# Optimization experiments

Measured on AMD Instinct MI355X. Metric: run time of the kernel, lower is better.

The kernel has to match this reference:

```python
import jax, jax.numpy as jnp
import numpy as np

N_NODES = 100000
N_EDGES = 3200000
F_IN, HIDDEN, N_CLASSES = 512, 256, 40


def setup_inputs() -> dict:
    key = jax.random.key(0)
    ks = jax.random.split(key, 8)
    x = jax.random.normal(ks[0], (N_NODES, F_IN), dtype=jnp.float32)
    edge_row = jax.random.randint(ks[1], (N_EDGES,), 0, N_NODES, dtype=jnp.int64)
    edge_col = jax.random.randint(ks[2], (N_EDGES,), 0, N_NODES, dtype=jnp.int64)
    edge_val = jax.random.uniform(ks[3], (N_EDGES,), dtype=jnp.float32)
    # Xavier-uniform-ish weights
    lim1 = float(np.sqrt(6.0 / (F_IN + HIDDEN)))
    lim2 = float(np.sqrt(6.0 / (HIDDEN + N_CLASSES)))
    W1 = jax.random.uniform(ks[4], (F_IN, HIDDEN), minval=-lim1, maxval=lim1, dtype=jnp.float32)
    b1 = jnp.zeros((HIDDEN,), dtype=jnp.float32)
    W2 = jax.random.uniform(ks[5], (HIDDEN, N_CLASSES), minval=-lim2, maxval=lim2, dtype=jnp.float32)
    b2 = jnp.zeros((N_CLASSES,), dtype=jnp.float32)
    return {"x": x, "edge_row": edge_row, "edge_col": edge_col, "edge_val": edge_val,
            "W1": W1, "b1": b1, "W2": W2, "b2": b2}


def _spmm(edge_row, edge_col, edge_val, h):
    # out[r] = sum_e val[e] * h[col[e]] for edges with row[e]==r  (a @ h)
    msg = edge_val[:, None] * h[edge_col]            # [E, F] gather + scale
    return jax.ops.segment_sum(msg, edge_row, num_segments=N_NODES)


def reference(x, edge_row, edge_col, edge_val, W1, b1, W2, b2):
    # Layer 1: dense mm -> spmm -> bias -> relu (dropout in eval mode = identity)
    h = _spmm(edge_row, edge_col, edge_val, x @ W1) + b1
    h = jax.nn.relu(h)
    # Layer 2: dense mm -> spmm -> bias
    logits = _spmm(edge_row, edge_col, edge_val, h @ W2) + b2
    return jax.nn.log_softmax(logits, axis=1)
```

## Files before the change

kernel.cpp:

```cpp
#include <hip/hip_runtime.h>
#include <math.h>

#define NN  100000
#define NE  3200000
#define FIN 512
#define HID 256
#define NC  40

#define NBUK 391
#define SPB  9472
#define BIN_BLOCKS 782
#define CHUNK 4096
#define COLMASK 0x1FFFF

typedef __attribute__((ext_vector_type(8))) short short8;
typedef __attribute__((ext_vector_type(4))) float f32x4;

__device__ inline float bf2f(unsigned short u) {
    unsigned int x = ((unsigned int)u) << 16;
    return __builtin_bit_cast(float, x);
}
__device__ inline unsigned short f2bfu(float f) {
    unsigned int x = __builtin_bit_cast(unsigned int, f);
    unsigned int r = (x + 0x7fffu + ((x >> 16) & 1u)) >> 16;
    return (unsigned short)r;
}
__device__ inline signed char q8(float v, float s) {
    int q = (int)rintf(v * s);
    q = max(-127, min(127, q));
    return (signed char)q;
}
__device__ inline unsigned cvtpk_bf16(float lo, float hi) {
    unsigned r;
    asm("v_cvt_pk_bf16_f32 %0, %1, %2" : "=v"(r) : "v"(lo), "v"(hi));
    return r;
}
__device__ inline float cub0(int r) { float f; asm("v_cvt_f32_ubyte0 %0, %1" : "=v"(f) : "v"(r)); return f; }
__device__ inline float cub1(int r) { float f; asm("v_cvt_f32_ubyte1 %0, %1" : "=v"(f) : "v"(r)); return f; }
__device__ inline float cub2(int r) { float f; asm("v_cvt_f32_ubyte2 %0, %1" : "=v"(f) : "v"(r)); return f; }
__device__ inline float cub3(int r) { float f; asm("v_cvt_f32_ubyte3 %0, %1" : "=v"(f) : "v"(r)); return f; }

__global__ __launch_bounds__(256) void k_prep(const float* __restrict__ W1, unsigned short* __restrict__ W1T,
                                              const float* __restrict__ W2, unsigned short* __restrict__ W2T,
                                              int* __restrict__ bcnt) {
    const int b = blockIdx.x;
    const int tid = threadIdx.x;
    if (b < 32) {
        unsigned short tmp[16];
#pragma unroll
        for (int kk = 0; kk < 16; kk++)
            tmp[kk] = f2bfu(W1[(size_t)(b * 16 + kk) * HID + tid]);
        unsigned short* dst = W1T + (size_t)tid * FIN + b * 16;
        *(short8*)dst = *(short8*)tmp;
        *(short8*)(dst + 8) = *(short8*)(tmp + 8);
    } else if (b < 80) {
        int n = b - 32;
        float v = (n < NC) ? W2[(size_t)tid * NC + n] : 0.f;
        W2T[(size_t)n * HID + tid] = f2bfu(v);
    } else {
        for (int i = tid; i < NBUK; i += 256) bcnt[i] = 0;
    }
}

__global__ __launch_bounds__(256) void k_bin(const int* __restrict__ er, const int* __restrict__ ec,
                                             const float* __restrict__ ev, int* __restrict__ bcnt,
                                             int2* __restrict__ spack) {
    __shared__ int hist[392];
    __shared__ int lscan[392];
    __shared__ int gbase[NBUK];
    __shared__ int lcur[NBUK];
    __shared__ int sm[256];
    __shared__ int2 ebuf[CHUNK];
    __shared__ unsigned short bbuf[CHUNK];
    const int tid = threadIdx.x;
    for (int i = tid; i < 392; i += 256) hist[i] = 0;
    for (int i = tid; i < NBUK; i += 256) lcur[i] = 0;
    __syncthreads();
    const int start = blockIdx.x * CHUNK;
    const int end = min(start + CHUNK, NE);
    const int n = end - start;
    for (int e = start + tid; e < end; e += 256)
        atomicAdd(&hist[er[e] >> 8], 1);
    __syncthreads();
    int a = (2 * tid < 392) ? hist[2 * tid] : 0;
    int b = (2 * tid + 1 < 392) ? hist[2 * tid + 1] : 0;
    int v = a + b;
    sm[tid] = v;
    __syncthreads();
    for (int off = 1; off < 256; off <<= 1) {
        int t2 = (tid >= off) ? sm[tid - off] : 0;
        __syncthreads();
        sm[tid] += t2;
        __syncthreads();
    }
    int ex = sm[tid] - v;
    if (2 * tid < 392) lscan[2 * tid] = ex;
    if (2 * tid + 1 < 392) lscan[2 * tid + 1] = ex + a;
    for (int i = tid; i < NBUK; i += 256) {
        int h = hist[i];
        gbase[i] = h ? atomicAdd(&bcnt[i], h) : 0;
    }
    __syncthreads();
    for (int e = start + tid; e < end; e += 256) {
        int r = er[e];
        int bk = r >> 8;
        int lpos = atomicAdd(&lcur[bk], 1);
        int pos = lscan[bk] + lpos;
        int2 p;
        p.x = ((r & 255) << 17) | ec[e];
        p.y = __builtin_bit_cast(int, ev[e]);
        ebuf[pos] = p;
        bbuf[pos] = (unsigned short)bk;
    }
    __syncthreads();
    for (int i = tid; i < n; i += 256) {
        int bk = bbuf[i];
        spack[(size_t)bk * SPB + gbase[bk] + (i - lscan[bk])] = ebuf[i];
    }
}

__global__ __launch_bounds__(256) void k_finecsr(const int2* __restrict__ spack, const int* __restrict__ bcnt,
                                                 int2* __restrict__ cpack,
                                                 int* __restrict__ row_beg, int* __restrict__ row_cnt) {
    __shared__ int cnt[256];
    __shared__ int sm[256];
    __shared__ int cur[256];
    int tid = threadIdx.x;
    int buk = blockIdx.x;
    size_t bb = (size_t)buk * SPB;
    int n = min(bcnt[buk], SPB);
    cnt[tid] = 0;
    __syncthreads();
    for (int i = tid; i < n; i += 256) {
        int lr = ((unsigned)spack[bb + i].x) >> 17;
        atomicAdd(&cnt[lr], 1);
    }
    __syncthreads();
    int v = cnt[tid];
    sm[tid] = v;
    __syncthreads();
    for (int off = 1; off < 256; off <<= 1) {
        int t = (tid >= off) ? sm[tid - off] : 0;
        __syncthreads();
        sm[tid] += t;
        __syncthreads();
    }
    int ex = sm[tid] - v;
    cur[tid] = ex;
    int grow = buk * 256 + tid;
    if (grow < NN) {
        row_beg[grow] = (int)bb + ex;
        row_cnt[grow] = v;
    }
    __syncthreads();
    for (int i = tid; i < n; i += 256) {
        int2 p = spack[bb + i];
        int lr = ((unsigned)p.x) >> 17;
        int pos = atomicAdd(&cur[lr], 1);
        int2 q;
        q.x = p.x & COLMASK;
        q.y = p.y;
        cpack[bb + pos] = q;
    }
}

__global__ __launch_bounds__(256, 4) void k_gemm1(const float* __restrict__ x, const unsigned short* __restrict__ W1T,
                                                  unsigned char* __restrict__ h1) {
    __shared__ unsigned short As[64][40];
    __shared__ unsigned short Bs[128][40];
    const int tid = threadIdx.x;
    const int row0 = (blockIdx.x >> 1) * 64;
    const int col0 = (blockIdx.x & 1) * 128;
    const int lane = tid & 63;
    const int w = tid >> 6;
    const int wr = (w >> 1) * 32;
    const int wc = (w & 1) * 64;
    const int m16 = lane & 15;
    const int quad = lane >> 4;

    const int arow = tid >> 2;
    const int akoff = (tid & 3) * 8;
    int gar = row0 + arow;
    if (gar >= NN) gar = NN - 1;
    const float* ax = x + (size_t)gar * FIN + akoff;
    const int brow = tid >> 1;
    const int bkoff = (tid & 1) * 16;
    const unsigned short* bw = W1T + (size_t)(col0 + brow) * FIN + bkoff;

    f32x4 acc[2][4];
#pragma unroll
    for (int i = 0; i < 2; i++)
#pragma unroll
        for (int j = 0; j < 4; j++) acc[i][j] = (f32x4){0.f, 0.f, 0.f, 0.f};

    float4 va0, va1;
    uint4 vb0, vb1;

#define G1_LOAD(tt)                                                        \
    {                                                                      \
        const float* ap = ax + (tt) * 32;                                  \
        va0 = *(const float4*)(ap);                                        \
        va1 = *(const float4*)(ap + 4);                                    \
        const unsigned short* bp = bw + (tt) * 32;                         \
        vb0 = *(const uint4*)(bp);                                         \
        vb1 = *(const uint4*)(bp + 8);                                     \
    }

#define G1_STORE()                                                         \
    {                                                                      \
        uint4 pa;                                                          \
        pa.x = cvtpk_bf16(va0.x, va0.y);                                   \
        pa.y = cvtpk_bf16(va0.z, va0.w);                                   \
        pa.z = cvtpk_bf16(va1.x, va1.y);                                   \
        pa.w = cvtpk_bf16(va1.z, va1.w);                                   \
        *(uint4*)(&As[arow][akoff]) = pa;                                  \
        *(uint4*)(&Bs[brow][bkoff]) = vb0;                                 \
        *(uint4*)(&Bs[brow][bkoff + 8]) = vb1;                             \
    }

    G1_LOAD(0)
    G1_STORE()
    __syncthreads();

    for (int t = 0; t < 16; ++t) {
        if (t < 15) G1_LOAD(t + 1)
        short8 af[2], bfr[4];
#pragma unroll
        for (int i = 0; i < 2; i++) af[i] = *(const short8*)(&As[wr + i * 16 + m16][quad * 8]);
#pragma unroll
        for (int j = 0; j < 4; j++) bfr[j] = *(const short8*)(&Bs[wc + j * 16 + m16][quad * 8]);
#pragma unroll
        for (int i = 0; i < 2; i++)
#pragma unroll
            for (int j = 0; j < 4; j++)
                acc[i][j] = __builtin_amdgcn_mfma_f32_16x16x32_bf16(af[i], bfr[j], acc[i][j], 0, 0, 0);
        if (t < 15) {
            __syncthreads();
            G1_STORE()
            __syncthreads();
        }
    }
#undef G1_LOAD
#undef G1_STORE

#pragma unroll
    for (int i = 0; i < 2; i++) {
#pragma unroll
        for (int r = 0; r < 4; r++) {
            int gr = row0 + wr + i * 16 + quad * 4 + r;
            if (gr < NN) {
#pragma unroll
                for (int j = 0; j < 4; j++) {
                    int c = col0 + wc + j * 16 + m16;
                    h1[(size_t)gr * HID + c] = (unsigned char)(q8(acc[i][j][r], 16.f) + 128);
                }
            }
        }
    }
}

__global__ __launch_bounds__(256) void k_spmm1(const unsigned char* __restrict__ h1,
                                               const int2* __restrict__ cpack,
                                               const int* __restrict__ row_beg, const int* __restrict__ row_cnt,
                                               const float* __restrict__ b1, unsigned short* __restrict__ a1) {
    const int lane = threadIdx.x & 63;
    const int row = (int)__builtin_amdgcn_readfirstlane(blockIdx.x * 4 + (threadIdx.x >> 6));
    if (row >= NN) return;
    const int beg = (int)__builtin_amdgcn_readfirstlane(row_beg[row]);
    const int cnt = (int)__builtin_amdgcn_readfirstlane(row_cnt[row]);
    const int end = beg + cnt;
    const int voff = lane * 4;
    float su[4] = {0.f, 0.f, 0.f, 0.f};
    float sv = 0.f;

    for (int e0 = beg; e0 < end; e0 += 16) {
        int2 p[16];
#pragma unroll
        for (int j = 0; j < 16; j++)
            p[j] = cpack[e0 + j];
        unsigned cb[16];
        float vv[16];
#pragma unroll
        for (int j = 0; j < 16; j++) {
            cb[j] = ((unsigned)p[j].x & COLMASK) << 8;
            vv[j] = (e0 + j) < end ? __builtin_bit_cast(float, p[j].y) : 0.f;
        }
        int g[16];
#pragma unroll
        for (int j = 0; j < 16; j++)
            g[j] = *(const int*)(h1 + (size_t)cb[j] + voff);
#pragma unroll
        for (int j = 0; j < 16; j++) {
            sv += vv[j];
            su[0] = fmaf(vv[j], cub0(g[j]), su[0]);
            su[1] = fmaf(vv[j], cub1(g[j]), su[1]);
            su[2] = fmaf(vv[j], cub2(g[j]), su[2]);
            su[3] = fmaf(vv[j], cub3(g[j]), su[3]);
        }
    }

    const int col = lane * 4;
    const float4 bb = *(const float4*)(b1 + col);
    ushort4 o;
    o.x = f2bfu(fmaxf(fmaf(0.0625f, fmaf(-128.f, sv, su[0]), bb.x), 0.f));
    o.y = f2bfu(fmaxf(fmaf(0.0625f, fmaf(-128.f, sv, su[1]), bb.y), 0.f));
    o.z = f2bfu(fmaxf(fmaf(0.0625f, fmaf(-128.f, sv, su[2]), bb.z), 0.f));
    o.w = f2bfu(fmaxf(fmaf(0.0625f, fmaf(-128.f, sv, su[3]), bb.w), 0.f));
    *(ushort4*)(a1 + (size_t)row * HID + col) = o;
}

__global__ __launch_bounds__(256) void k_gemm2(const unsigned short* __restrict__ a1,
                                               const unsigned short* __restrict__ W2T, unsigned char* __restrict__ h2) {
    const int tid = threadIdx.x;
    const int lane = tid & 63;
    const int w = tid >> 6;
    const int m16 = lane & 15;
    const int quad = lane >> 4;
    const int r0 = blockIdx.x * 256 + w * 64;

    f32x4 acc[4][3];
#pragma unroll
    for (int i = 0; i < 4; i++)
#pragma unroll
        for (int j = 0; j < 3; j++) acc[i][j] = (f32x4){0.f, 0.f, 0.f, 0.f};

    for (int k0 = 0; k0 < HID; k0 += 32) {
        short8 af[4], bfr[3];
#pragma unroll
        for (int i = 0; i < 4; i++) {
            int gr = r0 + i * 16 + m16;
            if (gr >= NN) gr = NN - 1;
            af[i] = *(const short8*)(a1 + (size_t)gr * HID + k0 + quad * 8);
        }
#pragma unroll
        for (int j = 0; j < 3; j++)
            bfr[j] = *(const short8*)(W2T + (size_t)(j * 16 + m16) * HID + k0 + quad * 8);
#pragma unroll
        for (int i = 0; i < 4; i++)
#pragma unroll
            for (int j = 0; j < 3; j++)
                acc[i][j] = __builtin_amdgcn_mfma_f32_16x16x32_bf16(af[i], bfr[j], acc[i][j], 0, 0, 0);
    }
#pragma unroll
    for (int i = 0; i < 4; i++) {
#pragma unroll
        for (int r = 0; r < 4; r++) {
            int gr = r0 + i * 16 + quad * 4 + r;
            if (gr < NN) {
#pragma unroll
                for (int j = 0; j < 3; j++) {
                    int c = j * 16 + m16;
                    if (c < NC) h2[(size_t)gr * 64 + c] = (unsigned char)(q8(acc[i][j][r], 4.f) + 128);
                }
            }
        }
    }
}

__global__ __launch_bounds__(256) void k_spmm2(const unsigned char* __restrict__ h2,
                                               const int2* __restrict__ cpack,
                                               const int* __restrict__ row_beg, const int* __restrict__ row_cnt,
                                               const float* __restrict__ b2, float* __restrict__ out) {
    const int lane = threadIdx.x & 63;
    const int slot = lane >> 4;
    const int t = lane & 15;
    const int row = (int)__builtin_amdgcn_readfirstlane(blockIdx.x * 4 + (threadIdx.x >> 6));
    if (row >= NN) return;
    const int beg = (int)__builtin_amdgcn_readfirstlane(row_beg[row]);
    const int cnt = (int)__builtin_amdgcn_readfirstlane(row_cnt[row]);
    const int end = beg + cnt;
    const int t4 = t * 4;
    float su[4] = {0.f, 0.f, 0.f, 0.f};
    float sv = 0.f;

    for (int e0 = beg; e0 < end; e0 += 32) {
        unsigned cb[8];
        float vs[8];
#pragma unroll
        for (int u = 0; u < 8; u++) {
            int idx = e0 + u * 4 + slot;
            int2 p = cpack[idx];
            cb[u] = ((unsigned)p.x & COLMASK) << 6;
            vs[u] = idx < end ? __builtin_bit_cast(float, p.y) : 0.f;
        }
        int g[8];
#pragma unroll
        for (int u = 0; u < 8; u++)
            g[u] = *(const int*)(h2 + (size_t)cb[u] + t4);
#pragma unroll
        for (int u = 0; u < 8; u++) {
            sv += vs[u];
            su[0] = fmaf(vs[u], cub0(g[u]), su[0]);
            su[1] = fmaf(vs[u], cub1(g[u]), su[1]);
            su[2] = fmaf(vs[u], cub2(g[u]), su[2]);
            su[3] = fmaf(vs[u], cub3(g[u]), su[3]);
        }
    }

#pragma unroll
    for (int i = 0; i < 4; i++) {
        su[i] += __shfl_xor(su[i], 16, 64);
        su[i] += __shfl_xor(su[i], 32, 64);
    }
    sv += __shfl_xor(sv, 16, 64);
    sv += __shfl_xor(sv, 32, 64);

    const bool act = t < 10;
    const int off = t4;
    const int boff = act ? off : 0;
    const float4 bb = *(const float4*)(b2 + boff);
    float acc[4];
    acc[0] = fmaf(0.25f, fmaf(-128.f, sv, su[0]), bb.x);
    acc[1] = fmaf(0.25f, fmaf(-128.f, sv, su[1]), bb.y);
    acc[2] = fmaf(0.25f, fmaf(-128.f, sv, su[2]), bb.z);
    acc[3] = fmaf(0.25f, fmaf(-128.f, sv, su[3]), bb.w);
    float mx = act ? fmaxf(fmaxf(acc[0], acc[1]), fmaxf(acc[2], acc[3])) : -INFINITY;
#pragma unroll
    for (int o = 1; o < 16; o <<= 1) mx = fmaxf(mx, __shfl_xor(mx, o, 16));
    float se = 0.f;
    if (act) {
#pragma unroll
        for (int i = 0; i < 4; i++) se += expf(acc[i] - mx);
    }
#pragma unroll
    for (int o = 1; o < 16; o <<= 1) se += __shfl_xor(se, o, 16);
    const float ls = logf(se);
    if (act && slot == 0) {
        float4 r;
        r.x = acc[0] - mx - ls;
        r.y = acc[1] - mx - ls;
        r.z = acc[2] - mx - ls;
        r.w = acc[3] - mx - ls;
        *(float4*)(out + (size_t)row * NC + off) = r;
    }
}

extern "C" void kernel_launch(void* const* d_in, const int* in_sizes, int n_in, void* d_out, int out_size,
                              void* d_ws, size_t ws_size, hipStream_t stream) {
    const float* x  = (const float*)d_in[0];
    const int*   er = (const int*)d_in[1];
    const int*   ec = (const int*)d_in[2];
    const float* ev = (const float*)d_in[3];
    const float* W1 = (const float*)d_in[4];
    const float* b1 = (const float*)d_in[5];
    const float* W2 = (const float*)d_in[6];
    const float* b2 = (const float*)d_in[7];
    float* out = (float*)d_out;
    char* ws = (char*)d_ws;

    int2*  spack       = (int2*)(ws + 0);
    unsigned char* h1  = (unsigned char*)(ws + 0);
    unsigned short* a1 = (unsigned short*)(ws + 29628416);
    unsigned char* h2  = (unsigned char*)(ws + 80828416);
    int2*  cpack       = (int2*)(ws + 87228416);
    int*   row_beg     = (int*)(ws + 116856832);
    int*   row_cnt     = (int*)(ws + 117256832);
    int*   bcnt        = (int*)(ws + 117656832);
    unsigned short* W1T = (unsigned short*)(ws + 117658880);
    unsigned short* W2T = (unsigned short*)(ws + 117921024);

    k_prep<<<81, 256, 0, stream>>>(W1, W1T, W2, W2T, bcnt);
    k_bin<<<BIN_BLOCKS, 256, 0, stream>>>(er, ec, ev, bcnt, spack);
    k_finecsr<<<NBUK, 256, 0, stream>>>(spack, bcnt, cpack, row_beg, row_cnt);
    k_gemm1<<<3126, 256, 0, stream>>>(x, W1T, h1);
    k_spmm1<<<NN / 4, 256, 0, stream>>>(h1, cpack, row_beg, row_cnt, b1, a1);
    k_gemm2<<<(NN + 255) / 256, 256, 0, stream>>>(a1, W2T, h2);
    k_spmm2<<<NN / 4, 256, 0, stream>>>(h2, cpack, row_beg, row_cnt, b2, out);
}
```

Before: 673.1 us.

## Fuse edge binning and GEMM1 into one launch with register-direct MFMA tiles

```diff
diff --git a/kernel.cpp b/kernel.cpp
--- a/kernel.cpp
+++ b/kernel.cpp
@@ -12,6 +12,7 @@
 #define BIN_BLOCKS 782
 #define CHUNK 4096
 #define COLMASK 0x1FFFF
+#define G1_BLOCKS 1563
 
 typedef __attribute__((ext_vector_type(8))) short short8;
 typedef __attribute__((ext_vector_type(4))) float f32x4;
@@ -62,60 +63,129 @@
     }
 }
 
-__global__ __launch_bounds__(256) void k_bin(const int* __restrict__ er, const int* __restrict__ ec,
-                                             const float* __restrict__ ev, int* __restrict__ bcnt,
-                                             int2* __restrict__ spack) {
-    __shared__ int hist[392];
-    __shared__ int lscan[392];
-    __shared__ int gbase[NBUK];
-    __shared__ int lcur[NBUK];
-    __shared__ int sm[256];
-    __shared__ int2 ebuf[CHUNK];
-    __shared__ unsigned short bbuf[CHUNK];
+__global__ __launch_bounds__(256) void k_fused(const float* __restrict__ x, const unsigned short* __restrict__ W1T,
+                                               unsigned char* __restrict__ h1,
+                                               const int* __restrict__ er, const int* __restrict__ ec,
+                                               const float* __restrict__ ev, int* __restrict__ bcnt,
+                                               int2* __restrict__ spack) {
     const int tid = threadIdx.x;
-    for (int i = tid; i < 392; i += 256) hist[i] = 0;
-    for (int i = tid; i < NBUK; i += 256) lcur[i] = 0;
-    __syncthreads();
-    const int start = blockIdx.x * CHUNK;
-    const int end = min(start + CHUNK, NE);
-    const int n = end - start;
-    for (int e = start + tid; e < end; e += 256)
-        atomicAdd(&hist[er[e] >> 8], 1);
-    __syncthreads();
-    int a = (2 * tid < 392) ? hist[2 * tid] : 0;
-    int b = (2 * tid + 1 < 392) ? hist[2 * tid + 1] : 0;
-    int v = a + b;
-    sm[tid] = v;
-    __syncthreads();
-    for (int off = 1; off < 256; off <<= 1) {
-        int t2 = (tid >= off) ? sm[tid - off] : 0;
-        __syncthreads();
-        sm[tid] += t2;
-        __syncthreads();
-    }
-    int ex = sm[tid] - v;
-    if (2 * tid < 392) lscan[2 * tid] = ex;
-    if (2 * tid + 1 < 392) lscan[2 * tid + 1] = ex + a;
-    for (int i = tid; i < NBUK; i += 256) {
-        int h = hist[i];
-        gbase[i] = h ? atomicAdd(&bcnt[i], h) : 0;
-    }
-    __syncthreads();
-    for (int e = start + tid; e < end; e += 256) {
-        int r = er[e];
-        int bk = r >> 8;
-        int lpos = atomicAdd(&lcur[bk], 1);
-        int pos = lscan[bk] + lpos;
-        int2 p;
-        p.x = ((r & 255) << 17) | ec[e];
-        p.y = __builtin_bit_cast(int, ev[e]);
-        ebuf[pos] = p;
-        bbuf[pos] = (unsigned short)bk;
-    }
-    __syncthreads();
-    for (int i = tid; i < n; i += 256) {
-        int bk = bbuf[i];
-        spack[(size_t)bk * SPB + gbase[bk] + (i - lscan[bk])] = ebuf[i];
+    if (blockIdx.x < BIN_BLOCKS) {
+        __shared__ int hist[392];
+        __shared__ int lscan[392];
+        __shared__ int gbase[NBUK];
+        __shared__ int lcur[NBUK];
+        __shared__ int sm[256];
+        __shared__ int2 ebuf[CHUNK];
+        __shared__ unsigned short bbuf[CHUNK];
+        for (int i = tid; i < 392; i += 256) hist[i] = 0;
+        for (int i = tid; i < NBUK; i += 256) lcur[i] = 0;
+        __syncthreads();
+        const int start = blockIdx.x * CHUNK;
+        const int end = min(start + CHUNK, NE);
+        const int n = end - start;
+        for (int e = start + tid; e < end; e += 256)
+            atomicAdd(&hist[er[e] >> 8], 1);
+        __syncthreads();
+        int a = (2 * tid < 392) ? hist[2 * tid] : 0;
+        int b = (2 * tid + 1 < 392) ? hist[2 * tid + 1] : 0;
+        int v = a + b;
+        sm[tid] = v;
+        __syncthreads();
+        for (int off = 1; off < 256; off <<= 1) {
+            int t2 = (tid >= off) ? sm[tid - off] : 0;
+            __syncthreads();
+            sm[tid] += t2;
+            __syncthreads();
+        }
+        int ex = sm[tid] - v;
+        if (2 * tid < 392) lscan[2 * tid] = ex;
+        if (2 * tid + 1 < 392) lscan[2 * tid + 1] = ex + a;
+        for (int i = tid; i < NBUK; i += 256) {
+            int h = hist[i];
+            gbase[i] = h ? atomicAdd(&bcnt[i], h) : 0;
+        }
+        __syncthreads();
+        for (int e = start + tid; e < end; e += 256) {
+            int r = er[e];
+            int bk = r >> 8;
+            int lpos = atomicAdd(&lcur[bk], 1);
+            int pos = lscan[bk] + lpos;
+            int2 p;
+            p.x = ((r & 255) << 17) | ec[e];
+            p.y = __builtin_bit_cast(int, ev[e]);
+            ebuf[pos] = p;
+            bbuf[pos] = (unsigned short)bk;
+        }
+        __syncthreads();
+        for (int i = tid; i < n; i += 256) {
+            int bk = bbuf[i];
+            spack[(size_t)bk * SPB + gbase[bk] + (i - lscan[bk])] = ebuf[i];
+        }
+        return;
+    }
+
+    const int gid = blockIdx.x - BIN_BLOCKS;
+    const int row0 = gid * 64;
+    const int lane = tid & 63;
+    const int w = tid >> 6;
+    const int col0 = w * 64;
+    const int m16 = lane & 15;
+    const int quad = lane >> 4;
+
+    const float* ap[4];
+#pragma unroll
+    for (int i = 0; i < 4; i++) {
+        int gr = row0 + i * 16 + m16;
+        if (gr >= NN) gr = NN - 1;
+        ap[i] = x + (size_t)gr * FIN + quad * 8;
+    }
+    const unsigned short* bp[4];
+#pragma unroll
+    for (int j = 0; j < 4; j++)
+        bp[j] = W1T + (size_t)(col0 + j * 16 + m16) * FIN + quad * 8;
+
+    f32x4 acc[4][4];
+#pragma unroll
+    for (int i = 0; i < 4; i++)
+#pragma unroll
+        for (int j = 0; j < 4; j++) acc[i][j] = (f32x4){0.f, 0.f, 0.f, 0.f};
+
+    for (int k0 = 0; k0 < FIN; k0 += 32) {
+        short8 af[4], bfr[4];
+#pragma unroll
+        for (int i = 0; i < 4; i++) {
+            const float4 lo = *(const float4*)(ap[i] + k0);
+            const float4 hi = *(const float4*)(ap[i] + k0 + 4);
+            uint4 pk;
+            pk.x = cvtpk_bf16(lo.x, lo.y);
+            pk.y = cvtpk_bf16(lo.z, lo.w);
+            pk.z = cvtpk_bf16(hi.x, hi.y);
+            pk.w = cvtpk_bf16(hi.z, hi.w);
+            af[i] = __builtin_bit_cast(short8, pk);
+        }
+#pragma unroll
+        for (int j = 0; j < 4; j++)
+            bfr[j] = *(const short8*)(bp[j] + k0);
+#pragma unroll
+        for (int i = 0; i < 4; i++)
+#pragma unroll
+            for (int j = 0; j < 4; j++)
+                acc[i][j] = __builtin_amdgcn_mfma_f32_16x16x32_bf16(af[i], bfr[j], acc[i][j], 0, 0, 0);
+    }
+
+#pragma unroll
+    for (int i = 0; i < 4; i++) {
+#pragma unroll
+        for (int r = 0; r < 4; r++) {
+            int gr = row0 + i * 16 + quad * 4 + r;
+            if (gr < NN) {
+#pragma unroll
+                for (int j = 0; j < 4; j++) {
+                    int c = col0 + j * 16 + m16;
+                    h1[(size_t)gr * HID + c] = (unsigned char)(q8(acc[i][j][r], 16.f) + 128);
+                }
+            }
+        }
     }
 }
 
@@ -164,101 +234,6 @@
     }
 }
 
-__global__ __launch_bounds__(256, 4) void k_gemm1(const float* __restrict__ x, const unsigned short* __restrict__ W1T,
-                                                  unsigned char* __restrict__ h1) {
-    __shared__ unsigned short As[64][40];
-    __shared__ unsigned short Bs[128][40];
-    const int tid = threadIdx.x;
-    const int row0 = (blockIdx.x >> 1) * 64;
-    const int col0 = (blockIdx.x & 1) * 128;
-    const int lane = tid & 63;
-    const int w = tid >> 6;
-    const int wr = (w >> 1) * 32;
-    const int wc = (w & 1) * 64;
-    const int m16 = lane & 15;
-    const int quad = lane >> 4;
-
-    const int arow = tid >> 2;
-    const int akoff = (tid & 3) * 8;
-    int gar = row0 + arow;
-    if (gar >= NN) gar = NN - 1;
-    const float* ax = x + (size_t)gar * FIN + akoff;
-    const int brow = tid >> 1;
-    const int bkoff = (tid & 1) * 16;
-    const unsigned short* bw = W1T + (size_t)(col0 + brow) * FIN + bkoff;
-
-    f32x4 acc[2][4];
-#pragma unroll
-    for (int i = 0; i < 2; i++)
-#pragma unroll
-        for (int j = 0; j < 4; j++) acc[i][j] = (f32x4){0.f, 0.f, 0.f, 0.f};
-
-    float4 va0, va1;
-    uint4 vb0, vb1;
-
-#define G1_LOAD(tt)                                                        \
-    {                                                                      \
-        const float* ap = ax + (tt) * 32;                                  \
-        va0 = *(const float4*)(ap);                                        \
-        va1 = *(const float4*)(ap + 4);                                    \
-        const unsigned short* bp = bw + (tt) * 32;                         \
-        vb0 = *(const uint4*)(bp);                                         \
-        vb1 = *(const uint4*)(bp + 8);                                     \
-    }
-
-#define G1_STORE()                                                         \
-    {                                                                      \
-        uint4 pa;                                                          \
-        pa.x = cvtpk_bf16(va0.x, va0.y);                                   \
-        pa.y = cvtpk_bf16(va0.z, va0.w);                                   \
-        pa.z = cvtpk_bf16(va1.x, va1.y);                                   \
-        pa.w = cvtpk_bf16(va1.z, va1.w);                                   \
-        *(uint4*)(&As[arow][akoff]) = pa;                                  \
-        *(uint4*)(&Bs[brow][bkoff]) = vb0;                                 \
-        *(uint4*)(&Bs[brow][bkoff + 8]) = vb1;                             \
-    }
-
-    G1_LOAD(0)
-    G1_STORE()
-    __syncthreads();
-
-    for (int t = 0; t < 16; ++t) {
-        if (t < 15) G1_LOAD(t + 1)
-        short8 af[2], bfr[4];
-#pragma unroll
-        for (int i = 0; i < 2; i++) af[i] = *(const short8*)(&As[wr + i * 16 + m16][quad * 8]);
-#pragma unroll
-        for (int j = 0; j < 4; j++) bfr[j] = *(const short8*)(&Bs[wc + j * 16 + m16][quad * 8]);
-#pragma unroll
-        for (int i = 0; i < 2; i++)
-#pragma unroll
-            for (int j = 0; j < 4; j++)
-                acc[i][j] = __builtin_amdgcn_mfma_f32_16x16x32_bf16(af[i], bfr[j], acc[i][j], 0, 0, 0);
-        if (t < 15) {
-            __syncthreads();
-            G1_STORE()
-            __syncthreads();
-        }
-    }
-#undef G1_LOAD
-#undef G1_STORE
-
-#pragma unroll
-    for (int i = 0; i < 2; i++) {
-#pragma unroll
-        for (int r = 0; r < 4; r++) {
-            int gr = row0 + wr + i * 16 + quad * 4 + r;
-            if (gr < NN) {
-#pragma unroll
-                for (int j = 0; j < 4; j++) {
-                    int c = col0 + wc + j * 16 + m16;
-                    h1[(size_t)gr * HID + c] = (unsigned char)(q8(acc[i][j][r], 16.f) + 128);
-                }
-            }
-        }
-    }
-}
-
 __global__ __launch_bounds__(256) void k_spmm1(const unsigned char* __restrict__ h1,
                                                const int2* __restrict__ cpack,
                                                const int* __restrict__ row_beg, const int* __restrict__ row_cnt,
@@ -449,20 +424,19 @@
     char* ws = (char*)d_ws;
 
     int2*  spack       = (int2*)(ws + 0);
-    unsigned char* h1  = (unsigned char*)(ws + 0);
-    unsigned short* a1 = (unsigned short*)(ws + 29628416);
-    unsigned char* h2  = (unsigned char*)(ws + 80828416);
-    int2*  cpack       = (int2*)(ws + 87228416);
-    int*   row_beg     = (int*)(ws + 116856832);
-    int*   row_cnt     = (int*)(ws + 117256832);
-    int*   bcnt        = (int*)(ws + 117656832);
-    unsigned short* W1T = (unsigned short*)(ws + 117658880);
-    unsigned short* W2T = (unsigned short*)(ws + 117921024);
+    unsigned short* a1 = (unsigned short*)(ws + 0);
+    unsigned char* h1  = (unsigned char*)(ws + 51200000);
+    unsigned char* h2  = (unsigned char*)(ws + 76800000);
+    int2*  cpack       = (int2*)(ws + 83200000);
+    int*   row_beg     = (int*)(ws + 112828416);
+    int*   row_cnt     = (int*)(ws + 113228416);
+    int*   bcnt        = (int*)(ws + 113628416);
+    unsigned short* W1T = (unsigned short*)(ws + 113630464);
+    unsigned short* W2T = (unsigned short*)(ws + 113892608);
 
     k_prep<<<81, 256, 0, stream>>>(W1, W1T, W2, W2T, bcnt);
-    k_bin<<<BIN_BLOCKS, 256, 0, stream>>>(er, ec, ev, bcnt, spack);
+    k_fused<<<BIN_BLOCKS + G1_BLOCKS, 256, 0, stream>>>(x, W1T, h1, er, ec, ev, bcnt, spack);
     k_finecsr<<<NBUK, 256, 0, stream>>>(spack, bcnt, cpack, row_beg, row_cnt);
-    k_gemm1<<<3126, 256, 0, stream>>>(x, W1T, h1);
     k_spmm1<<<NN / 4, 256, 0, stream>>>(h1, cpack, row_beg, row_cnt, b1, a1);
     k_gemm2<<<(NN + 255) / 256, 256, 0, stream>>>(a1, W2T, h2);
     k_spmm2<<<NN / 4, 256, 0, stream>>>(h2, cpack, row_beg, row_cnt, b2, out);
```

New measurement: 701.9 us. 4.3% more time.
